# Kernel optimization log

Measured on AMD Instinct MI355X. Metric: run time of the kernel, lower is better.

Reference implementation:

```python
import jax, jax.numpy as jnp
import numpy as np

B, C, H, W = 8, 16, 112, 112
K = 9            # NSCT subbands (level_map): 1 lowpass + 4 + 4 directional
FS = 9           # analysis/synthesis filter size
WIN = 7          # Swin window
DIM = K * C + C  # 160 = transformed + skip channels
HEADS = 5
HEAD_DIM = DIM // HEADS  # 32
MLP_DIM = 4 * DIM
SHIFTS = (0, WIN // 2)
NW = (H // WIN) * (W // WIN)
CONV_DN = ('NCHW', 'OIHW', 'NCHW')

def _rel_idx():
    co = np.stack(np.meshgrid(np.arange(WIN), np.arange(WIN), indexing='ij')).reshape(2, -1)
    rel = (co[:, :, None] - co[:, None, :]).transpose(1, 2, 0) + WIN - 1
    return rel[..., 0] * (2 * WIN - 1) + rel[..., 1]

REL_IDX = jnp.asarray(_rel_idx())  # [49,49]

def _attn_mask(shift):
    img = np.zeros((H, W))
    sl = (slice(0, -WIN), slice(-WIN, -shift), slice(-shift, None))
    c = 0
    for hs in sl:
        for ws in sl:
            img[hs, ws] = c; c += 1
    m = img.reshape(H // WIN, WIN, W // WIN, WIN).transpose(0, 2, 1, 3).reshape(NW, WIN * WIN)
    am = m[:, None, :] - m[:, :, None]
    return jnp.asarray(np.where(am != 0, -100.0, 0.0).astype(np.float32))  # [nW,49,49]

MASK1 = _attn_mask(SHIFTS[1])

def _ln(x, g, b, eps=1e-5):
    mu = x.mean(-1, keepdims=True)
    var = ((x - mu) ** 2).mean(-1, keepdims=True)
    return (x - mu) * jax.lax.rsqrt(var + eps) * g + b

def _win_part(x):
    Bb = x.shape[0]
    x = x.reshape(Bb, H // WIN, WIN, W // WIN, WIN, DIM).transpose(0, 1, 3, 2, 4, 5)
    return x.reshape(Bb * NW, WIN * WIN, DIM)

def _win_rev(xw, Bb):
    x = xw.reshape(Bb, H // WIN, W // WIN, WIN, WIN, DIM).transpose(0, 1, 3, 2, 4, 5)
    return x.reshape(Bb, H, W, DIM)

def _swin_block(x, shift, mask, ln1g, ln1b, qkvw, qkvb, projw, projb, rpb, ln2g, ln2b, w1, b1, w2, b2):
    Bb = x.shape[0]
    sc = x
    x = _ln(x, ln1g, ln1b)
    if shift:
        x = jnp.roll(x, (-shift, -shift), axis=(1, 2))
    xw = _win_part(x)                 # [B*nW,49,D]
    qkv = xw @ qkvw + qkvb            # [B*nW,49,3D]
    q, k, v = jnp.split(qkv, 3, axis=-1)
    heads = lambda t: t.reshape(-1, WIN * WIN, HEADS, HEAD_DIM).transpose(0, 2, 1, 3)
    q, k, v = heads(q), heads(k), heads(v)
    attn = jnp.einsum('whid,whjd->whij', q, k) * (HEAD_DIM ** -0.5)
    bias = rpb[REL_IDX].transpose(2, 0, 1)  # [heads,49,49]
    attn = attn + bias[None]
    if mask is not None:
        attn = attn.reshape(Bb, NW, HEADS, WIN * WIN, WIN * WIN) + mask[None, :, None]
        attn = attn.reshape(Bb * NW, HEADS, WIN * WIN, WIN * WIN)
    attn = jax.nn.softmax(attn, axis=-1)
    out = jnp.einsum('whij,whjd->whid', attn, v).transpose(0, 2, 1, 3).reshape(-1, WIN * WIN, DIM)
    out = out @ projw + projb
    x = _win_rev(out, Bb)
    if shift:
        x = jnp.roll(x, (shift, shift), axis=(1, 2))
    x = sc + x
    h = _ln(x, ln2g, ln2b)
    h = jax.nn.gelu(h @ w1 + b1) @ w2 + b2
    return x + h

def _forward(x, f_ana, f_syn, ln1g, ln1b, qkvw, qkvb, projw, projb, rpb, ln2g, ln2b, w1, b1, w2, b2, linw, linb, convw, convb):
    x2 = jax.nn.relu(x)
    # CT: per-channel 9-band nonsubsampled filter-bank decomposition (batched depthwise conv)
    sub = jax.lax.conv_general_dilated(x2.reshape(B * C, 1, H, W), f_ana, (1, 1), 'SAME', dimension_numbers=CONV_DN)
    x_trans = sub.reshape(B, C, K, H, W).transpose(0, 2, 1, 3, 4).reshape(B, K * C, H, W)  # subband-major channel order
    x3 = jnp.concatenate([x_trans, x2], axis=1).transpose(0, 2, 3, 1)  # [B,H,W,160]
    for i, (shift, mask) in enumerate(zip(SHIFTS, (None, MASK1))):
        x3 = _swin_block(x3, shift, mask, ln1g[i], ln1b[i], qkvw[i], qkvb[i], projw[i], projb[i], rpb[i], ln2g[i], ln2b[i], w1[i], b1[i], w2[i], b2[i])
    x3 = x3 @ linw + linb             # [B,H,W,144]
    y = x3.transpose(0, 3, 1, 2)      # [B,144,H,W]
    # ICT: per-channel synthesis filter-bank reconstruction
    ti = y.reshape(B, K, C, H, W).transpose(0, 2, 1, 3, 4).reshape(B * C, K, H, W)
    y_trans = jax.lax.conv_general_dilated(ti, f_syn, (1, 1), 'SAME', dimension_numbers=CONV_DN).reshape(B, C, H, W)
    yc = jnp.concatenate([y_trans, y], axis=1)  # [B,160,H,W]
    return jax.lax.conv_general_dilated(yc, convw, (1, 1), 'SAME', dimension_numbers=CONV_DN) + convb[None, :, None, None]

def setup_inputs() -> dict:
    key = jax.random.key(0)
    ks = jax.random.split(key, 12)
    s = 0.02
    return {
        'x': jax.random.normal(ks[0], (B, C, H, W), jnp.float32),
        'f_ana': jax.random.normal(ks[1], (K, 1, FS, FS), jnp.float32) * s,
        'f_syn': jax.random.normal(ks[2], (1, K, FS, FS), jnp.float32) * s,
        'ln1g': jnp.ones((2, DIM), jnp.float32),
        'ln1b': jnp.zeros((2, DIM), jnp.float32),
        'qkvw': jax.random.normal(ks[3], (2, DIM, 3 * DIM), jnp.float32) * s,
        'qkvb': jnp.zeros((2, 3 * DIM), jnp.float32),
        'projw': jax.random.normal(ks[4], (2, DIM, DIM), jnp.float32) * s,
        'projb': jnp.zeros((2, DIM), jnp.float32),
        'rpb': jax.random.normal(ks[5], (2, (2 * WIN - 1) ** 2, HEADS), jnp.float32) * s,
        'ln2g': jnp.ones((2, DIM), jnp.float32),
        'ln2b': jnp.zeros((2, DIM), jnp.float32),
        'w1': jax.random.normal(ks[6], (2, DIM, MLP_DIM), jnp.float32) * s,
        'b1': jnp.zeros((2, MLP_DIM), jnp.float32),
        'w2': jax.random.normal(ks[7], (2, MLP_DIM, DIM), jnp.float32) * s,
        'b2': jnp.zeros((2, DIM), jnp.float32),
        'linw': jax.random.normal(ks[8], (DIM, K * C), jnp.float32) * s,
        'linb': jnp.zeros((K * C,), jnp.float32),
        'convw': jax.random.normal(ks[9], (C, DIM, 1, 1), jnp.float32) * s,
        'convb': jnp.zeros((C,), jnp.float32),
    }

def reference(x, f_ana, f_syn, ln1g, ln1b, qkvw, qkvb, projw, projb, rpb, ln2g, ln2b, w1, b1, w2, b2, linw, linb, convw, convb):
    return _forward(x, f_ana, f_syn, ln1g, ln1b, qkvw, qkvb, projw, projb, rpb, ln2g, ln2b, w1, b1, w2, b2, linw, linb, convw, convb)
```

## Files before the change

kernel.cpp:

```cpp
#include <hip/hip_runtime.h>
#include <hip/hip_bf16.h>
#include <math.h>

#define BB 8
#define CC 16
#define HH 112
#define WW 112
#define KK 9
#define FS 9
#define WIN 7
#define DIM 160
#define HEADS 5
#define HDIM 32
#define MLPD 640
#define NWIN 256
#define NPOS (BB*HH*WW)

typedef __attribute__((ext_vector_type(8))) short short8;
typedef __attribute__((ext_vector_type(4))) float floatx4;

__device__ __forceinline__ unsigned short f2bf(float f) {
  union { float f; unsigned u; } v; v.f = f;
  unsigned r = v.u + 0x7fffu + ((v.u >> 16) & 1u);
  return (unsigned short)(r >> 16);
}
__device__ __forceinline__ float bf2f(unsigned short u) {
  union { unsigned u; float f; } v; v.u = ((unsigned)u) << 16;
  return v.f;
}
__device__ __forceinline__ float gelu_f(float a) {
  float z = 0.7978845608028654f * (a + 0.044715f * a * a * a);
  return a * __builtin_amdgcn_rcpf(1.f + __expf(-2.f * z));
}
__device__ __forceinline__ int orig_ch(int ch) {
  int c = ch / 10, k = ch - c * 10;
  return (k < 9) ? k * 16 + c : 144 + c;
}

__global__ __launch_bounds__(256) void ana_kernel(const float* __restrict__ x,
                                                  const float* __restrict__ fana,
                                                  float* __restrict__ x3) {
  __shared__ float tileS[8 * 576];
  __shared__ float fs[729];
  int tid = threadIdx.x;
  int blk = blockIdx.x;
  int b = blk / 98;
  int rem = blk - b * 98;
  int tile = rem >> 1;
  int half = rem & 1;
  int y0 = (tile / 7) * 16, x0 = (tile % 7) * 16;
  int c0 = half * 8;

  for (int i = tid; i < 729; i += 256) fs[i] = fana[i];
  for (int idx = tid; idx < 4608; idx += 256) {
    int cl = idx / 576, r = idx - cl * 576;
    int ly = r / 24, lx = r - ly * 24;
    int gy = y0 + ly - 4, gx = x0 + lx - 4;
    float v = 0.f;
    if (gy >= 0 && gy < HH && gx >= 0 && gx < WW)
      v = fmaxf(x[(((long)b * CC + (c0 + cl)) * HH + gy) * WW + gx], 0.f);
    tileS[idx] = v;
  }
  __syncthreads();

  int ty = tid >> 4, tx = tid & 15;
  long obase = (((long)b * HH + (y0 + ty)) * WW + (x0 + tx)) * DIM;
  for (int cg = 0; cg < 2; cg++) {
    float acc[4][9];
#pragma unroll
    for (int cl = 0; cl < 4; cl++)
#pragma unroll
      for (int k = 0; k < 9; k++) acc[cl][k] = 0.f;
    const float* ts0 = &tileS[(cg * 4 + 0) * 576];
    const float* ts1 = &tileS[(cg * 4 + 1) * 576];
    const float* ts2 = &tileS[(cg * 4 + 2) * 576];
    const float* ts3 = &tileS[(cg * 4 + 3) * 576];
    for (int ky = 0; ky < 9; ky++) {
      for (int kx = 0; kx < 9; kx++) {
        int toff = (ty + ky) * 24 + (tx + kx);
        float f[9];
#pragma unroll
        for (int k = 0; k < 9; k++) f[k] = fs[k * 81 + ky * 9 + kx];
        float v0 = ts0[toff], v1 = ts1[toff], v2 = ts2[toff], v3 = ts3[toff];
#pragma unroll
        for (int k = 0; k < 9; k++) {
          acc[0][k] += v0 * f[k];
          acc[1][k] += v1 * f[k];
          acc[2][k] += v2 * f[k];
          acc[3][k] += v3 * f[k];
        }
      }
    }
    int center = (ty + 4) * 24 + (tx + 4);
    const float* tsp[4] = {ts0, ts1, ts2, ts3};
#pragma unroll
    for (int cl = 0; cl < 4; cl++) {
      int c = c0 + cg * 4 + cl;
      float skip = tsp[cl][center];
      float2* dst = (float2*)&x3[obase + c * 10];
      dst[0] = make_float2(acc[cl][0], acc[cl][1]);
      dst[1] = make_float2(acc[cl][2], acc[cl][3]);
      dst[2] = make_float2(acc[cl][4], acc[cl][5]);
      dst[3] = make_float2(acc[cl][6], acc[cl][7]);
      dst[4] = make_float2(acc[cl][8], skip);
    }
  }
}

__device__ __forceinline__ int token_pos(int p, int shift) {
  int w = p / 49;
  int t = p - w * 49;
  int b = w >> 8;
  int wid = w & 255;
  int wi = wid >> 4, wj = wid & 15;
  int iy = t / 7, ix = t - (t / 7) * 7;
  int hy = (wi * 7 + iy + shift) % HH;
  int wx = (wj * 7 + ix + shift) % WW;
  return (b * HH + hy) * WW + wx;
}

__device__ __forceinline__ void pack_one(const float* __restrict__ src,
                                         unsigned short* __restrict__ dst,
                                         int nfcnt, int ncols, int nelems,
                                         int permK, int permN, int idx) {
  if (idx >= nelems) return;
  int j = idx & 7;
  int lane = (idx >> 3) & 63;
  int t = idx >> 9;
  int nf = t % nfcnt, ks = t / nfcnt;
  int k = ks * 32 + (lane >> 4) * 8 + j;
  int n = nf * 16 + (lane & 15);
  if (permK) k = orig_ch(k);
  if (permN) n = orig_ch(n);
  dst[idx] = f2bf(src[k * ncols + n]);
}

__global__ __launch_bounds__(256) void pack4_kernel(const float* __restrict__ qkvw,
                                                    const float* __restrict__ projw,
                                                    const float* __restrict__ w1,
                                                    const float* __restrict__ w2,
                                                    unsigned short* __restrict__ qkvf,
                                                    unsigned short* __restrict__ projf,
                                                    unsigned short* __restrict__ w1f,
                                                    unsigned short* __restrict__ w2f) {
  int blk = blockIdx.x, tid = threadIdx.x;
  if (blk < 300)      pack_one(qkvw,  qkvf,  30, 480, 76800,  1, 0, blk * 256 + tid);
  else if (blk < 400) pack_one(projw, projf, 10, 160, 25600,  0, 1, (blk - 300) * 256 + tid);
  else if (blk < 800) pack_one(w1,    w1f,   40, 640, 102400, 1, 0, (blk - 400) * 256 + tid);
  else                pack_one(w2,    w2f,   10, 160, 102400, 0, 1, (blk - 800) * 256 + tid);
}

__global__ __launch_bounds__(256) void pack1_kernel(const float* __restrict__ src,
                                                    unsigned short* __restrict__ dst,
                                                    int nfcnt, int ncols, int nelems,
                                                    int permK, int permN) {
  pack_one(src, dst, nfcnt, ncols, nelems, permK, permN, blockIdx.x * 256 + threadIdx.x);
}

__global__ __launch_bounds__(256) void qkv_mfma(const float* __restrict__ x3,
                                                const float* __restrict__ g,
                                                const float* __restrict__ bb,
                                                const unsigned short* __restrict__ qkvf,
                                                const float* __restrict__ qkvb,
                                                unsigned short* __restrict__ qkvbuf,
                                                int shift) {
  __shared__ unsigned short lnv[64 * 168];

  int tid = threadIdx.x;
  int p0 = blockIdx.x * 64;

  {
    int t = tid >> 2, sub = tid & 3;
    int pos = token_pos(p0 + t, shift);
    const float* row = x3 + (long)pos * 160 + sub * 40;
    float xv[40];
    float s1 = 0.f, s2 = 0.f;
#pragma unroll
    for (int m = 0; m < 40; m++) { float v = row[m]; xv[m] = v; s1 += v; s2 += v * v; }
    s1 += __shfl_xor(s1, 1); s2 += __shfl_xor(s2, 1);
    s1 += __shfl_xor(s1, 2); s2 += __shfl_xor(s2, 2);
    float mu = s1 * (1.f / 160.f);
    float rs = rsqrtf(s2 * (1.f / 160.f) - mu * mu + 1e-5f);
#pragma unroll
    for (int m = 0; m < 40; m++) {
      int c = sub * 40 + m;
      int oc = orig_ch(c);
      lnv[t * 168 + c] = f2bf((xv[m] - mu) * rs * g[oc] + bb[oc]);
    }
  }
  __syncthreads();

  int w = tid >> 6, lane = tid & 63, quad = lane >> 4, l16 = lane & 15;

#pragma unroll
  for (int half = 0; half < 2; half++) {
    floatx4 acc[15];
#pragma unroll
    for (int n = 0; n < 15; n++) acc[n] = (floatx4){0.f, 0.f, 0.f, 0.f};
    for (int ks = 0; ks < 5; ks++) {
      short8 a = *(const short8*)&lnv[(w * 16 + l16) * 168 + ks * 32 + quad * 8];
      const short8* bp = (const short8*)qkvf + (ks * 30 + half * 15) * 64 + lane;
#pragma unroll
      for (int n = 0; n < 15; n++)
        acc[n] = __builtin_amdgcn_mfma_f32_16x16x32_bf16(a, bp[n * 64], acc[n], 0, 0, 0);
    }
#pragma unroll
    for (int n = 0; n < 15; n++) {
      int col = (half * 15 + n) * 16 + l16;
      float bv = qkvb[col];
#pragma unroll
      for (int r = 0; r < 4; r++) {
        int tok = p0 + w * 16 + quad * 4 + r;
        qkvbuf[(long)tok * 480 + col] = f2bf(acc[n][r] + bv);
      }
    }
  }
}

__global__ __launch_bounds__(128) void attn_core(unsigned short* __restrict__ qkvbuf,
                                                 const float* __restrict__ rpb,
                                                 int shift) {
  __shared__ unsigned short qs[64 * 40];
  __shared__ unsigned short ks2[64 * 40];
  __shared__ unsigned short vT[32 * 68];
  __shared__ float pb[64 * 68];
  __shared__ float bias_s[169];

  int tid = threadIdx.x;
  int bid = blockIdx.x;
  int w = bid / 5, h = bid - (bid / 5) * 5;
  int wid = w & 255;
  int wi = wid >> 4, wj = wid & 15;
  long base = (long)w * 49 * 480;

  for (int idx = tid; idx < 784; idx += 128) {
    int m = idx / 392;
    int r = idx - m * 392;
    int t = r >> 3, d4 = r & 7;
    ushort4 u = *(const ushort4*)&qkvbuf[base + (long)t * 480 + m * 160 + h * 32 + d4 * 4];
    unsigned short* dst = m ? ks2 : qs;
    *(ushort4*)&dst[t * 40 + d4 * 4] = u;
  }
  for (int idx = tid; idx < 392; idx += 128) {
    int t = idx >> 3, d4 = idx & 7;
    ushort4 u = *(const ushort4*)&qkvbuf[base + (long)t * 480 + 320 + h * 32 + d4 * 4];
    vT[(d4 * 4 + 0) * 68 + t] = u.x;
    vT[(d4 * 4 + 1) * 68 + t] = u.y;
    vT[(d4 * 4 + 2) * 68 + t] = u.z;
    vT[(d4 * 4 + 3) * 68 + t] = u.w;
  }
  for (int idx = tid; idx < 32 * 19; idx += 128) {
    int n = idx / 19, k2 = idx - n * 19;
    vT[n * 68 + 49 + k2] = 0;
  }
  for (int i = tid; i < 169; i += 128) bias_s[i] = rpb[i * 5 + h];
  __syncthreads();

  int wv = tid >> 6, lane = tid & 63, quad = lane >> 4, l16 = lane & 15;

#pragma unroll
  for (int mf2 = 0; mf2 < 2; mf2++) {
    int mf = wv * 2 + mf2;
    short8 a = *(const short8*)&qs[(mf * 16 + l16) * 40 + quad * 8];
    int iy[4], ix[4], ai[4], bi[4];
#pragma unroll
    for (int r = 0; r < 4; r++) {
      int i = mf * 16 + quad * 4 + r;
      iy[r] = i / 7; ix[r] = i - iy[r] * 7;
      if (shift) {
        int hri = wi * 7 + iy[r], wri = wj * 7 + ix[r];
        ai[r] = hri < 105 ? 0 : (hri < 109 ? 1 : 2);
        bi[r] = wri < 105 ? 0 : (wri < 109 ? 1 : 2);
      }
    }
#pragma unroll
    for (int nf = 0; nf < 4; nf++) {
      short8 b = *(const short8*)&ks2[(nf * 16 + l16) * 40 + quad * 8];
      floatx4 c = (floatx4){0.f, 0.f, 0.f, 0.f};
      c = __builtin_amdgcn_mfma_f32_16x16x32_bf16(a, b, c, 0, 0, 0);
      int jj = nf * 16 + l16;
      if (jj < 49) {
        int jy = jj / 7, jx = jj - jy * 7;
        int aj = 0, bj2 = 0;
        if (shift) {
          int hrj = wi * 7 + jy, wrj = wj * 7 + jx;
          aj = hrj < 105 ? 0 : (hrj < 109 ? 1 : 2);
          bj2 = wrj < 105 ? 0 : (wrj < 109 ? 1 : 2);
        }
#pragma unroll
        for (int r = 0; r < 4; r++) {
          int i = mf * 16 + quad * 4 + r;
          int rel = (iy[r] - jy + 6) * 13 + (ix[r] - jx + 6);
          rel = rel > 168 ? 168 : rel;
          float s = c[r] * 0.17677669529663687f + bias_s[rel];
          if (shift && (ai[r] != aj || bi[r] != bj2)) s -= 100.f;
          pb[i * 68 + jj] = s;
        }
      } else {
#pragma unroll
        for (int r = 0; r < 4; r++) {
          int i = mf * 16 + quad * 4 + r;
          pb[i * 68 + jj] = 0.f;
        }
      }
    }
  }
  __syncthreads();

  if (tid < 49) {
    float* row = &pb[tid * 68];
    float m = -1e30f;
    for (int j = 0; j < 49; j++) m = fmaxf(m, row[j]);
    float sum = 0.f;
    for (int j = 0; j < 49; j++) { float e = __expf(row[j] - m); row[j] = e; sum += e; }
    float inv = 1.f / sum;
    for (int j = 0; j < 49; j++) row[j] *= inv;
  }
  __syncthreads();

  short8 bv[2][2];
#pragma unroll
  for (int nf = 0; nf < 2; nf++)
#pragma unroll
    for (int ks = 0; ks < 2; ks++)
      bv[nf][ks] = *(const short8*)&vT[(nf * 16 + l16) * 68 + ks * 32 + quad * 8];

#pragma unroll
  for (int mf2 = 0; mf2 < 2; mf2++) {
    int mf = wv * 2 + mf2;
    short8 ap[2];
#pragma unroll
    for (int ks = 0; ks < 2; ks++) {
      const float* pr = &pb[(mf * 16 + l16) * 68 + ks * 32 + quad * 8];
      float4 plo = *(const float4*)pr;
      float4 phi = *(const float4*)(pr + 4);
      short8 av;
      av[0] = (short)f2bf(plo.x); av[1] = (short)f2bf(plo.y);
      av[2] = (short)f2bf(plo.z); av[3] = (short)f2bf(plo.w);
      av[4] = (short)f2bf(phi.x); av[5] = (short)f2bf(phi.y);
      av[6] = (short)f2bf(phi.z); av[7] = (short)f2bf(phi.w);
      ap[ks] = av;
    }
#pragma unroll
    for (int nf = 0; nf < 2; nf++) {
      floatx4 c = (floatx4){0.f, 0.f, 0.f, 0.f};
      c = __builtin_amdgcn_mfma_f32_16x16x32_bf16(ap[0], bv[nf][0], c, 0, 0, 0);
      c = __builtin_amdgcn_mfma_f32_16x16x32_bf16(ap[1], bv[nf][1], c, 0, 0, 0);
#pragma unroll
      for (int r = 0; r < 4; r++) {
        int row = mf * 16 + quad * 4 + r;
        if (row < 49)
          qkvbuf[base + (long)row * 480 + h * 32 + nf * 16 + l16] = f2bf(c[r]);
      }
    }
  }
}

__global__ __launch_bounds__(256) void proj_mfma(const unsigned short* __restrict__ qkvbuf,
                                                 const unsigned short* __restrict__ projf,
                                                 const float* __restrict__ projb,
                                                 float* __restrict__ x3,
                                                 int shift) {
  __shared__ unsigned short ao[64 * 168];
  __shared__ int spos[64];
  int tid = threadIdx.x;
  int p0 = blockIdx.x * 64;
  if (tid < 64) spos[tid] = token_pos(p0 + tid, shift);
  for (int idx = tid; idx < 10240; idx += 256) {
    int t = idx / 160, ch = idx - t * 160;
    ao[t * 168 + ch] = qkvbuf[(long)(p0 + t) * 480 + ch];
  }
  __syncthreads();

  int w = tid >> 6, lane = tid & 63, quad = lane >> 4, l16 = lane & 15;
  floatx4 acc[10];
#pragma unroll
  for (int n = 0; n < 10; n++) acc[n] = (floatx4){0.f, 0.f, 0.f, 0.f};
  for (int ks = 0; ks < 5; ks++) {
    short8 a = *(const short8*)&ao[(w * 16 + l16) * 168 + ks * 32 + quad * 8];
    const short8* bp = (const short8*)projf + (ks * 10) * 64 + lane;
#pragma unroll
    for (int n = 0; n < 10; n++)
      acc[n] = __builtin_amdgcn_mfma_f32_16x16x32_bf16(a, bp[n * 64], acc[n], 0, 0, 0);
  }
#pragma unroll
  for (int n = 0; n < 10; n++) {
    int col = n * 16 + l16;
    float bv = projb[orig_ch(col)];
#pragma unroll
    for (int r = 0; r < 4; r++) {
      int tl = w * 16 + quad * 4 + r;
      long a = (long)spos[tl] * DIM + col;
      x3[a] = x3[a] + acc[n][r] + bv;
    }
  }
}

__global__ __launch_bounds__(256) void mlp_mfma(float* __restrict__ x3,
                                                const float* __restrict__ g,
                                                const float* __restrict__ bb,
                                                const unsigned short* __restrict__ w1f,
                                                const float* __restrict__ b1,
                                                const unsigned short* __restrict__ w2f,
                                                const float* __restrict__ b2) {
  __shared__ unsigned short lnv[32 * 168];
  __shared__ unsigned short h1s[32 * 648];

  int tid = threadIdx.x;
  long p0 = (long)blockIdx.x * 32;

  {
    int t = tid >> 3, sub = tid & 7;
    const float* row = x3 + (p0 + t) * 160 + sub * 20;
    float xv[20];
    float s1 = 0.f, s2 = 0.f;
#pragma unroll
    for (int m = 0; m < 20; m++) { float v = row[m]; xv[m] = v; s1 += v; s2 += v * v; }
#pragma unroll
    for (int m = 1; m < 8; m <<= 1) { s1 += __shfl_xor(s1, m); s2 += __shfl_xor(s2, m); }
    float mu = s1 * (1.f / 160.f);
    float rs = rsqrtf(s2 * (1.f / 160.f) - mu * mu + 1e-5f);
#pragma unroll
    for (int m = 0; m < 20; m++) {
      int c = sub * 20 + m;
      int oc = orig_ch(c);
      lnv[t * 168 + c] = f2bf((xv[m] - mu) * rs * g[oc] + bb[oc]);
    }
  }
  __syncthreads();

  int w = tid >> 6, lane = tid & 63, quad = lane >> 4, l16 = lane & 15;

  floatx4 acc[2][10];
#pragma unroll
  for (int mf = 0; mf < 2; mf++)
#pragma unroll
    for (int n = 0; n < 10; n++) acc[mf][n] = (floatx4){0.f, 0.f, 0.f, 0.f};

  for (int ks = 0; ks < 5; ks++) {
    short8 a0 = *(const short8*)&lnv[l16 * 168 + ks * 32 + quad * 8];
    short8 a1 = *(const short8*)&lnv[(16 + l16) * 168 + ks * 32 + quad * 8];
    const short8* bp = (const short8*)w1f + (ks * 40 + w * 10) * 64 + lane;
#pragma unroll
    for (int n = 0; n < 10; n++) {
      short8 bf = bp[n * 64];
      acc[0][n] = __builtin_amdgcn_mfma_f32_16x16x32_bf16(a0, bf, acc[0][n], 0, 0, 0);
      acc[1][n] = __builtin_amdgcn_mfma_f32_16x16x32_bf16(a1, bf, acc[1][n], 0, 0, 0);
    }
  }

#pragma unroll
  for (int mf = 0; mf < 2; mf++)
#pragma unroll
    for (int n = 0; n < 10; n++) {
      int col = w * 160 + n * 16 + l16;
      float bv = b1[col];
#pragma unroll
      for (int r = 0; r < 4; r++) {
        int tok = mf * 16 + quad * 4 + r;
        h1s[tok * 648 + col] = f2bf(gelu_f(acc[mf][n][r] + bv));
      }
    }
  __syncthreads();

  int mf = w & 1, nb = (w >> 1) * 5;
  floatx4 acc2[5];
#pragma unroll
  for (int n = 0; n < 5; n++) acc2[n] = (floatx4){0.f, 0.f, 0.f, 0.f};
  for (int ks = 0; ks < 20; ks++) {
    short8 a = *(const short8*)&h1s[(mf * 16 + l16) * 648 + ks * 32 + quad * 8];
    const short8* bp = (const short8*)w2f + (ks * 10 + nb) * 64 + lane;
#pragma unroll
    for (int n = 0; n < 5; n++)
      acc2[n] = __builtin_amdgcn_mfma_f32_16x16x32_bf16(a, bp[n * 64], acc2[n], 0, 0, 0);
  }

#pragma unroll
  for (int n = 0; n < 5; n++) {
    int col = (nb + n) * 16 + l16;
    float bv = b2[orig_ch(col)];
#pragma unroll
    for (int r = 0; r < 4; r++) {
      int tok = mf * 16 + quad * 4 + r;
      long a = (p0 + tok) * 160 + col;
      x3[a] = x3[a] + acc2[n][r] + bv;
    }
  }
}

__global__ __launch_bounds__(256) void lin_mfma(const float* __restrict__ x3,
                                                const unsigned short* __restrict__ linf,
                                                const float* __restrict__ linb,
                                                float* __restrict__ yp) {
  __shared__ unsigned short xs[64 * 168];
  int tid = threadIdx.x;
  int p0 = blockIdx.x * 64;

  for (int idx = tid; idx < 5120; idx += 256) {
    int t = idx / 80, c2 = idx - t * 80;
    float2 v = *(const float2*)&x3[((long)(p0 + t)) * 160 + c2 * 2];
    *(ushort2*)&xs[t * 168 + c2 * 2] = make_ushort2(f2bf(v.x), f2bf(v.y));
  }
  __syncthreads();

  int w = tid >> 6, lane = tid & 63, quad = lane >> 4, l16 = lane & 15;
  floatx4 acc[9];
#pragma unroll
  for (int n = 0; n < 9; n++) acc[n] = (floatx4){0.f, 0.f, 0.f, 0.f};
  for (int ks = 0; ks < 5; ks++) {
    short8 a = *(const short8*)&xs[(w * 16 + l16) * 168 + ks * 32 + quad * 8];
    const short8* bp = (const short8*)linf + (ks * 9) * 64 + lane;
#pragma unroll
    for (int n = 0; n < 9; n++)
      acc[n] = __builtin_amdgcn_mfma_f32_16x16x32_bf16(a, bp[n * 64], acc[n], 0, 0, 0);
  }
#pragma unroll
  for (int n = 0; n < 9; n++) {
    int col = n * 16 + l16;
    float bv = linb[col];
    float4 o = make_float4(acc[n][0] + bv, acc[n][1] + bv, acc[n][2] + bv, acc[n][3] + bv);
    *(float4*)&yp[(long)col * NPOS + p0 + w * 16 + quad * 4] = o;
  }
}

__global__ __launch_bounds__(256) void syn_kernel(const float* __restrict__ yp,
                                                  const float* __restrict__ fsyn,
                                                  float* __restrict__ yt) {
  __shared__ float tileS[24 * 120];
  __shared__ float fsl[729];
  int tid = threadIdx.x;
  int blk = blockIdx.x;
  int tile = blk % 7;
  int c = (blk / 7) % 16;
  int b = blk / 112;
  int ty0 = tile * 16;

  for (int i = tid; i < 729; i += 256) fsl[i] = fsyn[i];

  int ty = tid >> 4, txg = tid & 15;
  float acc[7];
#pragma unroll
  for (int w = 0; w < 7; w++) acc[w] = 0.f;

  for (int k = 0; k < 9; k++) {
    const float* plane = yp + (long)(k * 16 + c) * NPOS + (long)b * HH * WW;
    __syncthreads();
    for (int idx = tid; idx < 2880; idx += 256) {
      int ly = idx / 120, lx = idx - ly * 120;
      int gy = ty0 + ly - 4, gx = lx - 4;
      float v = 0.f;
      if (gy >= 0 && gy < HH && gx >= 0 && gx < WW) v = plane[gy * WW + gx];
      tileS[idx] = v;
    }
    __syncthreads();

#pragma unroll
    for (int ky = 0; ky < 9; ky++) {
      const float* row = &tileS[(ty + ky) * 120 + txg * 7];
      float rr[15];
#pragma unroll
      for (int i = 0; i < 15; i++) rr[i] = row[i];
      const float* fk = &fsl[k * 81 + ky * 9];
#pragma unroll
      for (int kx = 0; kx < 9; kx++) {
        float f = fk[kx];
#pragma unroll
        for (int w = 0; w < 7; w++) acc[w] += rr[kx + w] * f;
      }
    }
  }

  long obase = (long)c * NPOS + ((long)b * HH + (ty0 + ty)) * WW + txg * 7;
#pragma unroll
  for (int w = 0; w < 7; w++) yt[obase + w] = acc[w];
}

__global__ __launch_bounds__(256) void final_kernel(const float* __restrict__ yt,
                                                    const float* __restrict__ yp,
                                                    const float* __restrict__ convw,
                                                    const float* __restrict__ convb,
                                                    float* __restrict__ out) {
  long pos = (long)blockIdx.x * 256 + threadIdx.x;
  if (pos >= NPOS) return;
  int b = (int)(pos / (HH * WW));
  int hw = (int)(pos - (long)b * HH * WW);

  float acc[16];
#pragma unroll
  for (int co = 0; co < 16; co++) acc[co] = convb[co];
  for (int c = 0; c < 16; c++) {
    float v = yt[(long)c * NPOS + pos];
#pragma unroll
    for (int co = 0; co < 16; co++) acc[co] += v * convw[co * 160 + c];
  }
  for (int j = 0; j < 144; j++) {
    float v = yp[(long)j * NPOS + pos];
#pragma unroll
    for (int co = 0; co < 16; co++) acc[co] += v * convw[co * 160 + 16 + j];
  }
#pragma unroll
  for (int co = 0; co < 16; co++)
    out[(((long)b * 16 + co) * HH * WW) + hw] = acc[co];
}

extern "C" void kernel_launch(void* const* d_in, const int* in_sizes, int n_in,
                              void* d_out, int out_size, void* d_ws, size_t ws_size,
                              hipStream_t stream) {
  const float* x     = (const float*)d_in[0];
  const float* fana  = (const float*)d_in[1];
  const float* fsyn  = (const float*)d_in[2];
  const float* ln1g  = (const float*)d_in[3];
  const float* ln1b  = (const float*)d_in[4];
  const float* qkvw  = (const float*)d_in[5];
  const float* qkvb  = (const float*)d_in[6];
  const float* projw = (const float*)d_in[7];
  const float* projb = (const float*)d_in[8];
  const float* rpb   = (const float*)d_in[9];
  const float* ln2g  = (const float*)d_in[10];
  const float* ln2b  = (const float*)d_in[11];
  const float* w1    = (const float*)d_in[12];
  const float* b1    = (const float*)d_in[13];
  const float* w2    = (const float*)d_in[14];
  const float* b2    = (const float*)d_in[15];
  const float* linw  = (const float*)d_in[16];
  const float* linb  = (const float*)d_in[17];
  const float* convw = (const float*)d_in[18];
  const float* convb = (const float*)d_in[19];
  float* out = (float*)d_out;

  char* ws = (char*)d_ws;
  float* x3 = (float*)ws;
  char* region2 = ws + 64225280;
  unsigned short* qkvbuf = (unsigned short*)region2;
  unsigned short* packs  = (unsigned short*)(region2 + 96337920);
  unsigned short* qkvf = packs;
  unsigned short* projf = packs + 76800;
  unsigned short* w1f   = packs + 102400;
  unsigned short* w2f   = packs + 204800;
  unsigned short* linf  = packs + 307200;
  float* yp = (float*)region2;
  float* yt = (float*)ws;

  ana_kernel<<<BB * 98, 256, 0, stream>>>(x, fana, x3);
  pack1_kernel<<<90, 256, 0, stream>>>(linw, linf, 9, 144, 23040, 1, 0);
  for (int i = 0; i < 2; i++) {
    int shift = i ? (WIN / 2) : 0;
    pack4_kernel<<<1200, 256, 0, stream>>>(qkvw + i * 76800, projw + i * 25600,
                                           w1 + i * 102400, w2 + i * 102400,
                                           qkvf, projf, w1f, w2f);
    qkv_mfma<<<NPOS / 64, 256, 0, stream>>>(x3, ln1g + i * 160, ln1b + i * 160,
                                            qkvf, qkvb + i * 480, qkvbuf, shift);
    attn_core<<<BB * NWIN * HEADS, 128, 0, stream>>>(qkvbuf, rpb + i * 169 * 5, shift);
    proj_mfma<<<NPOS / 64, 256, 0, stream>>>(qkvbuf, projf, projb + i * 160, x3, shift);
    mlp_mfma<<<NPOS / 32, 256, 0, stream>>>(x3, ln2g + i * 160, ln2b + i * 160,
                                            w1f, b1 + i * 640, w2f, b2 + i * 160);
  }
  lin_mfma<<<NPOS / 64, 256, 0, stream>>>(x3, linf, linb, yp);
  syn_kernel<<<BB * 16 * 7, 256, 0, stream>>>(yp, fsyn, yt);
  final_kernel<<<(NPOS + 255) / 256, 256, 0, stream>>>(yt, yp, convw, convb, out);
}
```

Before: 1.020 ms.

## Fuse attention projection and MLP into one kernel per 32-token tile

Merges the projection GEMM with residual add and the LN2+MLP kernel into a single kernel. The post-projection residual is held in shared memory in fp32, which avoids a global write and re-read of x3 and one launch per block. The MLP output is written back to the original (unshifted) positions through the spos mapping. The cost is a larger shared-memory footprint per block and a half-width 32-token tile for the projection GEMM.

```diff
diff --git a/kernel.cpp b/kernel.cpp
--- a/kernel.cpp
+++ b/kernel.cpp
@@ -356,62 +356,62 @@
   }
 }
 
-__global__ __launch_bounds__(256) void proj_mfma(const unsigned short* __restrict__ qkvbuf,
-                                                 const unsigned short* __restrict__ projf,
-                                                 const float* __restrict__ projb,
-                                                 float* __restrict__ x3,
-                                                 int shift) {
-  __shared__ unsigned short ao[64 * 168];
-  __shared__ int spos[64];
+__global__ __launch_bounds__(256) void projmlp_mfma(const unsigned short* __restrict__ qkvbuf,
+                                                    const unsigned short* __restrict__ projf,
+                                                    const float* __restrict__ projb,
+                                                    float* __restrict__ x3,
+                                                    const float* __restrict__ g,
+                                                    const float* __restrict__ bb,
+                                                    const unsigned short* __restrict__ w1f,
+                                                    const float* __restrict__ b1,
+                                                    const unsigned short* __restrict__ w2f,
+                                                    const float* __restrict__ b2,
+                                                    int shift) {
+  __shared__ float xs[32 * 168];
+  __shared__ unsigned short u16[32 * 168];
+  __shared__ unsigned short h1s[32 * 648];
+  __shared__ int spos[32];
+
   int tid = threadIdx.x;
-  int p0 = blockIdx.x * 64;
-  if (tid < 64) spos[tid] = token_pos(p0 + tid, shift);
-  for (int idx = tid; idx < 10240; idx += 256) {
+  int p0 = blockIdx.x * 32;
+  if (tid < 32) spos[tid] = token_pos(p0 + tid, shift);
+  for (int idx = tid; idx < 5120; idx += 256) {
     int t = idx / 160, ch = idx - t * 160;
-    ao[t * 168 + ch] = qkvbuf[(long)(p0 + t) * 480 + ch];
+    u16[t * 168 + ch] = qkvbuf[(long)(p0 + t) * 480 + ch];
   }
   __syncthreads();
 
   int w = tid >> 6, lane = tid & 63, quad = lane >> 4, l16 = lane & 15;
-  floatx4 acc[10];
-#pragma unroll
-  for (int n = 0; n < 10; n++) acc[n] = (floatx4){0.f, 0.f, 0.f, 0.f};
+  int mf = w & 1, nb = (w >> 1) * 5;
+
+  floatx4 pacc[5];
+#pragma unroll
+  for (int n = 0; n < 5; n++) pacc[n] = (floatx4){0.f, 0.f, 0.f, 0.f};
   for (int ks = 0; ks < 5; ks++) {
-    short8 a = *(const short8*)&ao[(w * 16 + l16) * 168 + ks * 32 + quad * 8];
-    const short8* bp = (const short8*)projf + (ks * 10) * 64 + lane;
-#pragma unroll
-    for (int n = 0; n < 10; n++)
-      acc[n] = __builtin_amdgcn_mfma_f32_16x16x32_bf16(a, bp[n * 64], acc[n], 0, 0, 0);
-  }
-#pragma unroll
-  for (int n = 0; n < 10; n++) {
-    int col = n * 16 + l16;
+    short8 a = *(const short8*)&u16[(mf * 16 + l16) * 168 + ks * 32 + quad * 8];
+    const short8* bp = (const short8*)projf + (ks * 10 + nb) * 64 + lane;
+#pragma unroll
+    for (int n = 0; n < 5; n++)
+      pacc[n] = __builtin_amdgcn_mfma_f32_16x16x32_bf16(a, bp[n * 64], pacc[n], 0, 0, 0);
+  }
+  __syncthreads();
+
+#pragma unroll
+  for (int n = 0; n < 5; n++) {
+    int col = (nb + n) * 16 + l16;
     float bv = projb[orig_ch(col)];
 #pragma unroll
     for (int r = 0; r < 4; r++) {
-      int tl = w * 16 + quad * 4 + r;
-      long a = (long)spos[tl] * DIM + col;
-      x3[a] = x3[a] + acc[n][r] + bv;
-    }
-  }
-}
-
-__global__ __launch_bounds__(256) void mlp_mfma(float* __restrict__ x3,
-                                                const float* __restrict__ g,
-                                                const float* __restrict__ bb,
-                                                const unsigned short* __restrict__ w1f,
-                                                const float* __restrict__ b1,
-                                                const unsigned short* __restrict__ w2f,
-                                                const float* __restrict__ b2) {
-  __shared__ unsigned short lnv[32 * 168];
-  __shared__ unsigned short h1s[32 * 648];
-
-  int tid = threadIdx.x;
-  long p0 = (long)blockIdx.x * 32;
+      int tok = mf * 16 + quad * 4 + r;
+      float xv = x3[(long)spos[tok] * 160 + col] + pacc[n][r] + bv;
+      xs[tok * 168 + col] = xv;
+    }
+  }
+  __syncthreads();
 
   {
     int t = tid >> 3, sub = tid & 7;
-    const float* row = x3 + (p0 + t) * 160 + sub * 20;
+    const float* row = &xs[t * 168 + sub * 20];
     float xv[20];
     float s1 = 0.f, s2 = 0.f;
 #pragma unroll
@@ -424,22 +424,20 @@
     for (int m = 0; m < 20; m++) {
       int c = sub * 20 + m;
       int oc = orig_ch(c);
-      lnv[t * 168 + c] = f2bf((xv[m] - mu) * rs * g[oc] + bb[oc]);
-    }
-  }
-  __syncthreads();
-
-  int w = tid >> 6, lane = tid & 63, quad = lane >> 4, l16 = lane & 15;
+      u16[t * 168 + c] = f2bf((xv[m] - mu) * rs * g[oc] + bb[oc]);
+    }
+  }
+  __syncthreads();
 
   floatx4 acc[2][10];
 #pragma unroll
-  for (int mf = 0; mf < 2; mf++)
-#pragma unroll
-    for (int n = 0; n < 10; n++) acc[mf][n] = (floatx4){0.f, 0.f, 0.f, 0.f};
+  for (int m2 = 0; m2 < 2; m2++)
+#pragma unroll
+    for (int n = 0; n < 10; n++) acc[m2][n] = (floatx4){0.f, 0.f, 0.f, 0.f};
 
   for (int ks = 0; ks < 5; ks++) {
-    short8 a0 = *(const short8*)&lnv[l16 * 168 + ks * 32 + quad * 8];
-    short8 a1 = *(const short8*)&lnv[(16 + l16) * 168 + ks * 32 + quad * 8];
+    short8 a0 = *(const short8*)&u16[l16 * 168 + ks * 32 + quad * 8];
+    short8 a1 = *(const short8*)&u16[(16 + l16) * 168 + ks * 32 + quad * 8];
     const short8* bp = (const short8*)w1f + (ks * 40 + w * 10) * 64 + lane;
 #pragma unroll
     for (int n = 0; n < 10; n++) {
@@ -450,20 +448,19 @@
   }
 
 #pragma unroll
-  for (int mf = 0; mf < 2; mf++)
+  for (int m2 = 0; m2 < 2; m2++)
 #pragma unroll
     for (int n = 0; n < 10; n++) {
       int col = w * 160 + n * 16 + l16;
       float bv = b1[col];
 #pragma unroll
       for (int r = 0; r < 4; r++) {
-        int tok = mf * 16 + quad * 4 + r;
-        h1s[tok * 648 + col] = f2bf(gelu_f(acc[mf][n][r] + bv));
+        int tok = m2 * 16 + quad * 4 + r;
+        h1s[tok * 648 + col] = f2bf(gelu_f(acc[m2][n][r] + bv));
       }
     }
   __syncthreads();
 
-  int mf = w & 1, nb = (w >> 1) * 5;
   floatx4 acc2[5];
 #pragma unroll
   for (int n = 0; n < 5; n++) acc2[n] = (floatx4){0.f, 0.f, 0.f, 0.f};
@@ -482,8 +479,7 @@
 #pragma unroll
     for (int r = 0; r < 4; r++) {
       int tok = mf * 16 + quad * 4 + r;
-      long a = (p0 + tok) * 160 + col;
-      x3[a] = x3[a] + acc2[n][r] + bv;
+      x3[(long)spos[tok] * 160 + col] = xs[tok * 168 + col] + acc2[n][r] + bv;
     }
   }
 }
@@ -651,9 +647,10 @@
     qkv_mfma<<<NPOS / 64, 256, 0, stream>>>(x3, ln1g + i * 160, ln1b + i * 160,
                                             qkvf, qkvb + i * 480, qkvbuf, shift);
     attn_core<<<BB * NWIN * HEADS, 128, 0, stream>>>(qkvbuf, rpb + i * 169 * 5, shift);
-    proj_mfma<<<NPOS / 64, 256, 0, stream>>>(qkvbuf, projf, projb + i * 160, x3, shift);
-    mlp_mfma<<<NPOS / 32, 256, 0, stream>>>(x3, ln2g + i * 160, ln2b + i * 160,
-                                            w1f, b1 + i * 640, w2f, b2 + i * 160);
+    projmlp_mfma<<<NPOS / 32, 256, 0, stream>>>(qkvbuf, projf, projb + i * 160, x3,
+                                                ln2g + i * 160, ln2b + i * 160,
+                                                w1f, b1 + i * 640, w2f, b2 + i * 160,
+                                                shift);
   }
   lin_mfma<<<NPOS / 64, 256, 0, stream>>>(x3, linf, linb, yp);
   syn_kernel<<<BB * 16 * 7, 256, 0, stream>>>(yp, fsyn, yt);
```

Measured after the change: 1.012 ms. No clear change (-0.8%).
